# Optimization experiments

Hardware: AMD Instinct MI355X
Metric: run time of the kernel (lower is better)

Reference implementation:

```python
import jax, jax.numpy as jnp
import numpy as np

N, E = 100000, 800000
C_IN, C_OUT, OUT_SIZE = 64, 64, 8


def setup_inputs() -> dict:
    key = jax.random.key(0)
    ks = jax.random.split(key, 20)
    s = 0.05
    def p(k, shape):
        return jax.random.normal(k, shape, jnp.float32) * s
    return {
        "x": jax.random.normal(ks[0], (N, C_IN), jnp.float32),
        "edge_index": jax.random.randint(ks[1], (2, E), 0, N),
        "edge_weight": jax.random.uniform(ks[2], (E,), jnp.float32),
        # GCNConv weights (applied as x @ W), one per gate
        "conv_z_W": p(ks[3], (C_IN, C_OUT)), "conv_z_b": p(ks[4], (C_OUT,)),
        "conv_r_W": p(ks[5], (C_IN, C_OUT)), "conv_r_b": p(ks[6], (C_OUT,)),
        "conv_h_W": p(ks[7], (C_IN, C_OUT)), "conv_h_b": p(ks[8], (C_OUT,)),
        # GRU gate linears: Linear(2*C_OUT, C_OUT)
        "lin_z_W": p(ks[9], (2 * C_OUT, C_OUT)), "lin_z_b": p(ks[10], (C_OUT,)),
        "lin_r_W": p(ks[11], (2 * C_OUT, C_OUT)), "lin_r_b": p(ks[12], (C_OUT,)),
        "lin_h_W": p(ks[13], (2 * C_OUT, C_OUT)), "lin_h_b": p(ks[14], (C_OUT,)),
        # output head Linear(C_OUT, OUT_SIZE)
        "head_W": p(ks[15], (C_OUT, OUT_SIZE)), "head_b": p(ks[16], (OUT_SIZE,)),
    }


def _tgcn_forward(x, edge_index, edge_weight,
                  conv_z_W, conv_z_b, conv_r_W, conv_r_b, conv_h_W, conv_h_b,
                  lin_z_W, lin_z_b, lin_r_W, lin_r_b, lin_h_W, lin_h_b,
                  head_W, head_b):
    n = x.shape[0]
    src, dst = edge_index[0], edge_index[1]
    # GCN normalization with self-loops (fill_value = 1)
    loop = jnp.arange(n)
    src_f = jnp.concatenate([src, loop])
    dst_f = jnp.concatenate([dst, loop])
    ew_f = jnp.concatenate([edge_weight, jnp.ones((n,), x.dtype)])
    deg = jax.ops.segment_sum(ew_f, dst_f, num_segments=n)
    deg_safe = jnp.where(deg > 0, deg, 1.0)
    dinv = jnp.where(deg > 0, jax.lax.rsqrt(deg_safe), 0.0)
    norm = dinv[src_f] * ew_f * dinv[dst_f]  # [E + N]

    def gcn(W, b):
        msg = (x @ W)[src_f] * norm[:, None]          # gather + scale
        return jax.ops.segment_sum(msg, dst_f, num_segments=n) + b  # scatter-add

    H = jnp.zeros((n, conv_z_W.shape[1]), x.dtype)
    Z = jax.nn.sigmoid(jnp.concatenate([gcn(conv_z_W, conv_z_b), H], -1) @ lin_z_W + lin_z_b)
    R = jax.nn.sigmoid(jnp.concatenate([gcn(conv_r_W, conv_r_b), H], -1) @ lin_r_W + lin_r_b)
    H_tilde = jnp.tanh(jnp.concatenate([gcn(conv_h_W, conv_h_b), H * R], -1) @ lin_h_W + lin_h_b)
    H = Z * H + (1.0 - Z) * H_tilde
    return jax.nn.relu(H) @ head_W + head_b


def reference(x, edge_index, edge_weight,
              conv_z_W, conv_z_b, conv_r_W, conv_r_b, conv_h_W, conv_h_b,
              lin_z_W, lin_z_b, lin_r_W, lin_r_b, lin_h_W, lin_h_b,
              head_W, head_b):
    return _tgcn_forward(x, edge_index, edge_weight,
                         conv_z_W, conv_z_b, conv_r_W, conv_r_b, conv_h_W, conv_h_b,
                         lin_z_W, lin_z_b, lin_r_W, lin_r_b, lin_h_W, lin_h_b,
                         head_W, head_b)
```

## Files before the change

### kernel.cpp

```cpp
#include <hip/hip_runtime.h>

#define NN 100000
#define NE 800000
#define C 64
#define NB1 391
#define NTILES 3125
#define MAXDEG 40
#define WBITS 15
#define WMASK 32767u
#define WSCALE 32768.0f


__global__ void ell_build(const int* __restrict__ src, const int* __restrict__ dst,
                          const float* __restrict__ ew,
                          unsigned* __restrict__ cnt, unsigned* __restrict__ ell) {
    int e = blockIdx.x * 256 + threadIdx.x;
    if (e >= NE) return;
    int s = src[e], d = dst[e];
    float w = ew[e];
    unsigned w15 = (unsigned)(w * WSCALE + 0.5f);
    if (w15 > WMASK) w15 = WMASK;
    unsigned pos = atomicAdd(&cnt[d], 1u);
    if (pos < MAXDEG) ell[d * MAXDEG + pos] = ((unsigned)s << WBITS) | w15;
}

__global__ void finalize_ell(const unsigned* __restrict__ cnt,
                             const unsigned* __restrict__ ell,
                             float* __restrict__ dinv) {
    int t = blockIdx.x * 256 + threadIdx.x;
    int n = t >> 6, l = t & 63;
    if (n >= NN) return;
    int k = min((int)cnt[n], MAXDEG);
    float w = (l < k) ? (float)(ell[n * MAXDEG + l] & WMASK) * (1.0f / WSCALE) : 0.0f;
    for (int off = 32; off; off >>= 1) w += __shfl_xor(w, off, 64);
    if (l == 0) dinv[n] = rsqrtf(w + 1.0f);
}

__global__ __launch_bounds__(256) void gather_ell(
    const float* __restrict__ x, const float* __restrict__ dinv,
    const unsigned* __restrict__ cnt, const unsigned* __restrict__ ell,
    float* __restrict__ agg) {
    int t = blockIdx.x * 256 + threadIdx.x;
    int n = t >> 6, c = t & 63;
    if (n >= NN) return;
    float di = dinv[n];
    float acc = x[n * C + c] * di * di;
    int k = min((int)cnt[n], MAXDEG);
    const unsigned* base = ell + (size_t)n * MAXDEG;
    int e = 0;
    for (; e + 7 < k; e += 8) {
        uint4 q0 = *(const uint4*)(base + e);
        uint4 q1 = *(const uint4*)(base + e + 4);
        int s0 = q0.x >> WBITS, s1 = q0.y >> WBITS, s2 = q0.z >> WBITS, s3 = q0.w >> WBITS;
        int s4 = q1.x >> WBITS, s5 = q1.y >> WBITS, s6 = q1.z >> WBITS, s7 = q1.w >> WBITS;
        float x0 = x[s0 * C + c], x1 = x[s1 * C + c], x2 = x[s2 * C + c], x3 = x[s3 * C + c];
        float x4 = x[s4 * C + c], x5 = x[s5 * C + c], x6 = x[s6 * C + c], x7 = x[s7 * C + c];
        float d0 = dinv[s0], d1 = dinv[s1], d2 = dinv[s2], d3 = dinv[s3];
        float d4 = dinv[s4], d5 = dinv[s5], d6 = dinv[s6], d7 = dinv[s7];
        acc += x0 * (d0 * (float)(q0.x & WMASK) * (di * (1.0f / WSCALE)));
        acc += x1 * (d1 * (float)(q0.y & WMASK) * (di * (1.0f / WSCALE)));
        acc += x2 * (d2 * (float)(q0.z & WMASK) * (di * (1.0f / WSCALE)));
        acc += x3 * (d3 * (float)(q0.w & WMASK) * (di * (1.0f / WSCALE)));
        acc += x4 * (d4 * (float)(q1.x & WMASK) * (di * (1.0f / WSCALE)));
        acc += x5 * (d5 * (float)(q1.y & WMASK) * (di * (1.0f / WSCALE)));
        acc += x6 * (d6 * (float)(q1.z & WMASK) * (di * (1.0f / WSCALE)));
        acc += x7 * (d7 * (float)(q1.w & WMASK) * (di * (1.0f / WSCALE)));
    }
    if (e + 3 < k) {
        uint4 q0 = *(const uint4*)(base + e);
        int s0 = q0.x >> WBITS, s1 = q0.y >> WBITS, s2 = q0.z >> WBITS, s3 = q0.w >> WBITS;
        float x0 = x[s0 * C + c], x1 = x[s1 * C + c], x2 = x[s2 * C + c], x3 = x[s3 * C + c];
        float d0 = dinv[s0], d1 = dinv[s1], d2 = dinv[s2], d3 = dinv[s3];
        acc += x0 * (d0 * (float)(q0.x & WMASK) * (di * (1.0f / WSCALE)));
        acc += x1 * (d1 * (float)(q0.y & WMASK) * (di * (1.0f / WSCALE)));
        acc += x2 * (d2 * (float)(q0.z & WMASK) * (di * (1.0f / WSCALE)));
        acc += x3 * (d3 * (float)(q0.w & WMASK) * (di * (1.0f / WSCALE)));
        e += 4;
    }
    for (; e < k; ++e) {
        unsigned u = base[e];
        int s = u >> WBITS;
        acc += x[s * C + c] * (dinv[s] * (float)(u & WMASK) * (di * (1.0f / WSCALE)));
    }
    agg[t] = acc;
}


__global__ void count_deg(const int* __restrict__ dst, const float* __restrict__ ew,
                          float* __restrict__ deg, int* __restrict__ cnt) {
    int e = blockIdx.x * blockDim.x + threadIdx.x;
    if (e < NE) {
        int d = dst[e];
        atomicAdd(&deg[d], ew[e]);
        atomicAdd(&cnt[d], 1);
    }
}

__global__ void scan1(const int* __restrict__ cnt, int* __restrict__ row,
                      int* __restrict__ bsum) {
    __shared__ int s[256];
    int tid = threadIdx.x;
    int gid = blockIdx.x * 256 + tid;
    int v = (gid < NN) ? cnt[gid] : 0;
    s[tid] = v;
    for (int off = 1; off < 256; off <<= 1) {
        __syncthreads();
        int t = (tid >= off) ? s[tid - off] : 0;
        __syncthreads();
        s[tid] += t;
    }
    if (gid < NN) row[gid] = s[tid] - v;
    if (tid == 255) bsum[blockIdx.x] = s[255];
}

__global__ void scan2(const int* __restrict__ bsum, int* __restrict__ bo) {
    __shared__ int s[512];
    int tid = threadIdx.x;
    int v = (tid < NB1) ? bsum[tid] : 0;
    s[tid] = v;
    for (int off = 1; off < 512; off <<= 1) {
        __syncthreads();
        int t = (tid >= off) ? s[tid - off] : 0;
        __syncthreads();
        s[tid] += t;
    }
    if (tid < NB1) bo[tid] = s[tid] - v;
}

__global__ void finalize(int* __restrict__ row, const int* __restrict__ bo,
                         int* __restrict__ cursor, const float* __restrict__ deg,
                         float* __restrict__ dinv) {
    int gid = blockIdx.x * 256 + threadIdx.x;
    if (gid < NN) {
        int r = row[gid] + bo[gid >> 8];
        row[gid] = r;
        cursor[gid] = r;
        dinv[gid] = rsqrtf(deg[gid] + 1.0f);
        if (gid == 0) row[NN] = NE;
    }
}

__global__ void bucket(const int* __restrict__ src, const int* __restrict__ dst,
                       const float* __restrict__ ew, const float* __restrict__ dinv,
                       int* __restrict__ cursor, int2* __restrict__ edata) {
    int e = blockIdx.x * 256 + threadIdx.x;
    if (e < NE) {
        int s = src[e], d = dst[e];
        float nrm = dinv[s] * ew[e] * dinv[d];
        int pos = atomicAdd(&cursor[d], 1);
        edata[pos] = make_int2(s, __float_as_int(nrm));
    }
}

__global__ void gather(const float* __restrict__ x, const float* __restrict__ dinv,
                       const int* __restrict__ row, const int2* __restrict__ edata,
                       float* __restrict__ agg) {
    int t = blockIdx.x * 256 + threadIdx.x;
    int n = t >> 6, c = t & 63;
    if (n >= NN) return;
    float di = dinv[n];
    float acc = x[n * C + c] * di * di;
    int e = row[n], end = row[n + 1];
    for (; e + 1 < end; e += 2) {
        int2 e0 = edata[e], e1 = edata[e + 1];
        acc += x[e0.x * C + c] * __int_as_float(e0.y);
        acc += x[e1.x * C + c] * __int_as_float(e1.y);
    }
    if (e < end) {
        int2 e0 = edata[e];
        acc += x[e0.x * C + c] * __int_as_float(e0.y);
    }
    agg[t] = acc;
}

__global__ void fuse_weights(const float* __restrict__ Wz, const float* __restrict__ bz,
                             const float* __restrict__ Lz, const float* __restrict__ lzb,
                             const float* __restrict__ Wh, const float* __restrict__ bh,
                             const float* __restrict__ Lh, const float* __restrict__ lhb,
                             float* __restrict__ WzF, float* __restrict__ bzF,
                             float* __restrict__ WhF, float* __restrict__ bhF) {
    int t = blockIdx.x * blockDim.x + threadIdx.x;
    if (t < 4096) {
        int i = t >> 6, j = t & 63;
        float s = 0.0f;
#pragma unroll 8
        for (int k = 0; k < 64; k++) s += Wz[i * 64 + k] * Lz[k * 64 + j];
        WzF[t] = s;
    } else if (t < 8192) {
        int u = t - 4096;
        int i = u >> 6, j = u & 63;
        float s = 0.0f;
#pragma unroll 8
        for (int k = 0; k < 64; k++) s += Wh[i * 64 + k] * Lh[k * 64 + j];
        WhF[u] = s;
    } else if (t < 8256) {
        int j = t - 8192;
        float s = lzb[j];
#pragma unroll 8
        for (int k = 0; k < 64; k++) s += bz[k] * Lz[k * 64 + j];
        bzF[j] = s;
    } else if (t < 8320) {
        int j = t - 8256;
        float s = lhb[j];
#pragma unroll 8
        for (int k = 0; k < 64; k++) s += bh[k] * Lh[k * 64 + j];
        bhF[j] = s;
    }
}

__global__ __launch_bounds__(256) void gate_head(
    const float* __restrict__ agg,
    const float* __restrict__ WzF, const float* __restrict__ bzF,
    const float* __restrict__ WhF, const float* __restrict__ bhF,
    const float* __restrict__ headW, const float* __restrict__ headb,
    float* __restrict__ out) {
    __shared__ float sWz[4096];
    __shared__ float sWh[4096];
    __shared__ float sHead[512];
    __shared__ float sbz[64], sbh[64], shb[8];
    __shared__ float sAgg[32][64];
    __shared__ float sRh[32][65];

    int tid = threadIdx.x;
    for (int i = tid; i < 4096; i += 256) { sWz[i] = WzF[i]; sWh[i] = WhF[i]; }
    for (int i = tid; i < 512; i += 256) sHead[i] = headW[i];
    if (tid < 64) { sbz[tid] = bzF[tid]; sbh[tid] = bhF[tid]; }
    if (tid < 8) shb[tid] = headb[tid];
    __syncthreads();

    int j = tid & 63;
    int g = tid >> 6;
    int nl = tid >> 3;
    int j8 = tid & 7;

    for (int tIdx = blockIdx.x; tIdx < NTILES; tIdx += gridDim.x) {
        int n0 = tIdx * 32;
        for (int i = tid; i < 32 * 64; i += 256)
            sAgg[i >> 6][i & 63] = agg[n0 * 64 + i];
        __syncthreads();

        float az[8], ah[8];
#pragma unroll
        for (int l = 0; l < 8; l++) { az[l] = sbz[j]; ah[l] = sbh[j]; }
#pragma unroll 8
        for (int k = 0; k < 64; k++) {
            float wz = sWz[k * 64 + j];
            float wh = sWh[k * 64 + j];
#pragma unroll
            for (int l = 0; l < 8; l++) {
                float a = sAgg[g * 8 + l][k];
                az[l] += a * wz;
                ah[l] += a * wh;
            }
        }
#pragma unroll
        for (int l = 0; l < 8; l++) {
            float z = 1.0f / (1.0f + __expf(-az[l]));
            float ac = fminf(fmaxf(ah[l], -15.0f), 15.0f);
            float e2 = __expf(2.0f * ac);
            float ht = (e2 - 1.0f) / (e2 + 1.0f);
            float h = (1.0f - z) * ht;
            sRh[g * 8 + l][j] = fmaxf(h, 0.0f);
        }
        __syncthreads();

        float s = shb[j8];
#pragma unroll 8
        for (int k = 0; k < 64; k++) s += sRh[nl][k] * sHead[k * 8 + j8];
        out[(n0 + nl) * 8 + j8] = s;
        __syncthreads();
    }
}


__global__ void deg_scatter(const int* __restrict__ dst, const float* __restrict__ ew,
                            float* __restrict__ deg) {
    int e = blockIdx.x * blockDim.x + threadIdx.x;
    if (e < NE) atomicAdd(&deg[dst[e]], ew[e]);
}

__global__ void node_init(const float* __restrict__ x, const float* __restrict__ deg,
                          float* __restrict__ dinv, float* __restrict__ agg) {
    int t = blockIdx.x * blockDim.x + threadIdx.x;
    if (t >= NN * C) return;
    int n = t >> 6;
    float d = deg[n] + 1.0f;
    float di = rsqrtf(d);
    if ((t & 63) == 0) dinv[n] = di;
    agg[t] = x[t] * (di * di);
}

__global__ void edge_scatter(const int* __restrict__ src, const int* __restrict__ dst,
                             const float* __restrict__ ew, const float* __restrict__ dinv,
                             const float* __restrict__ x, float* __restrict__ agg) {
    int t = blockIdx.x * blockDim.x + threadIdx.x;
    int e = t >> 6;
    int c = t & 63;
    if (e >= NE) return;
    int s = src[e];
    int d = dst[e];
    float nrm = dinv[s] * ew[e] * dinv[d];
    atomicAdd(&agg[d * C + c], x[s * C + c] * nrm);
}

extern "C" void kernel_launch(void* const* d_in, const int* in_sizes, int n_in,
                              void* d_out, int out_size, void* d_ws, size_t ws_size,
                              hipStream_t stream) {
    const float* x     = (const float*)d_in[0];
    const int*   ei    = (const int*)d_in[1];
    const float* ew    = (const float*)d_in[2];
    const float* Wz    = (const float*)d_in[3];
    const float* bz    = (const float*)d_in[4];
    const float* Wh    = (const float*)d_in[7];
    const float* bh    = (const float*)d_in[8];
    const float* Lz    = (const float*)d_in[9];
    const float* lzb   = (const float*)d_in[10];
    const float* Lh    = (const float*)d_in[13];
    const float* lhb   = (const float*)d_in[14];
    const float* headW = (const float*)d_in[15];
    const float* headb = (const float*)d_in[16];
    float* out = (float*)d_out;

    const int* src = ei;
    const int* dst = ei + NE;

    float* agg    = (float*)d_ws;
    float* dinv   = agg + (size_t)NN * C;
    float* WzF    = dinv + NN;
    float* WhF    = WzF + 4096;
    float* bzF    = WhF + 4096;
    float* bhF    = bzF + 64;
    float* tail   = bhF + 64;

    unsigned* cnt_u = (unsigned*)tail;
    unsigned* ell   = cnt_u + NN;
    size_t need_ell = (size_t)(tail - (float*)d_ws) * 4 + (size_t)NN * 4
                    + (size_t)NN * MAXDEG * 4;

    float* deg    = tail;
    int*   cnt    = (int*)(deg + NN);
    int*   row    = cnt + NN;
    int*   cursor = row + NN + 1;
    int*   bsum   = cursor + NN;
    int*   bo     = bsum + 512;
    int2*  edata  = (int2*)(bo + 512 + 1);
    size_t need_csr  = ((size_t)(bo + 512 + 1 - (int*)d_ws) + 2 * (size_t)NE) * 4;
    size_t need_base = (size_t)((int*)cnt - (int*)d_ws) * 4;

    fuse_weights<<<33, 256, 0, stream>>>(Wz, bz, Lz, lzb, Wh, bh, Lh, lhb,
                                         WzF, bzF, WhF, bhF);

    if (ws_size >= need_ell) {
        hipMemsetAsync(cnt_u, 0, NN * sizeof(unsigned), stream);
        ell_build<<<(NE + 255) / 256, 256, 0, stream>>>(src, dst, ew, cnt_u, ell);
        finalize_ell<<<(NN * 64 + 255) / 256, 256, 0, stream>>>(cnt_u, ell, dinv);
        gather_ell<<<(NN * C) / 256, 256, 0, stream>>>(x, dinv, cnt_u, ell, agg);
        gate_head<<<768, 256, 0, stream>>>(agg, WzF, bzF, WhF, bhF, headW, headb, out);
    } else if (ws_size >= need_csr) {
        hipMemsetAsync(deg, 0, NN * sizeof(float), stream);
        hipMemsetAsync(cnt, 0, NN * sizeof(int), stream);
        count_deg<<<(NE + 255) / 256, 256, 0, stream>>>(dst, ew, deg, cnt);
        scan1<<<NB1, 256, 0, stream>>>(cnt, row, bsum);
        scan2<<<1, 512, 0, stream>>>(bsum, bo);
        finalize<<<NB1, 256, 0, stream>>>(row, bo, cursor, deg, dinv);
        bucket<<<(NE + 255) / 256, 256, 0, stream>>>(src, dst, ew, dinv, cursor, edata);
        gather<<<(NN * C) / 256, 256, 0, stream>>>(x, dinv, row, edata, agg);
        gate_head<<<768, 256, 0, stream>>>(agg, WzF, bzF, WhF, bhF, headW, headb, out);
    } else if (ws_size >= need_base) {
        hipMemsetAsync(deg, 0, NN * sizeof(float), stream);
        deg_scatter<<<(NE + 255) / 256, 256, 0, stream>>>(dst, ew, deg);
        node_init<<<(NN * C + 255) / 256, 256, 0, stream>>>(x, deg, dinv, agg);
        edge_scatter<<<(NE * C) / 256, 256, 0, stream>>>(src, dst, ew, dinv, x, agg);
        gate_head<<<768, 256, 0, stream>>>(agg, WzF, bzF, WhF, bhF, headW, headb, out);
    }
}
```

Before: 255.8 us.

## Gather bf16 copy of node features and fuse prep work into one kernel

Adds a prep kernel that converts x to bf16 and also does the weight fusion and the zeroing of the per-node counters, replacing a separate kernel launch and a memset. The gather then reads 2-byte features instead of 4-byte ones, halving the bytes per random neighbour row fetch. The cost is an extra full pass over x (read 25.6MB, write 12.8MB) plus lower precision in the aggregated features. It also needs more workspace, so the ELL path may fall back if the workspace is too small.

```diff
diff --git a/kernel.cpp b/kernel.cpp
--- a/kernel.cpp
+++ b/kernel.cpp
@@ -9,6 +9,71 @@
 #define WBITS 15
 #define WMASK 32767u
 #define WSCALE 32768.0f
+
+#define PREP_CONV 6250
+#define PREP_FUSE 33
+#define PREP_ZERO 98
+#define PREP_BLOCKS (PREP_CONV + PREP_FUSE + PREP_ZERO)
+
+__device__ __forceinline__ unsigned short f2bf(float f) {
+    unsigned b = __float_as_uint(f);
+    return (unsigned short)((b + 0x7FFFu + ((b >> 16) & 1u)) >> 16);
+}
+__device__ __forceinline__ float bf2f(unsigned short u) {
+    return __uint_as_float((unsigned)u << 16);
+}
+
+__global__ __launch_bounds__(256) void prep(
+    const float* __restrict__ x, unsigned short* __restrict__ xb,
+    const float* __restrict__ Wz, const float* __restrict__ bz,
+    const float* __restrict__ Lz, const float* __restrict__ lzb,
+    const float* __restrict__ Wh, const float* __restrict__ bh,
+    const float* __restrict__ Lh, const float* __restrict__ lhb,
+    float* __restrict__ WzF, float* __restrict__ bzF,
+    float* __restrict__ WhF, float* __restrict__ bhF,
+    unsigned* __restrict__ cnt) {
+    int b = blockIdx.x;
+    if (b < PREP_CONV) {
+        int i = (b * 256 + threadIdx.x) * 4;
+        float4 v = *(const float4*)(x + i);
+        ushort4 o;
+        o.x = f2bf(v.x); o.y = f2bf(v.y); o.z = f2bf(v.z); o.w = f2bf(v.w);
+        *(ushort4*)(xb + i) = o;
+    } else if (b < PREP_CONV + PREP_FUSE) {
+        int t = (b - PREP_CONV) * 256 + threadIdx.x;
+        if (t < 4096) {
+            int i = t >> 6, j = t & 63;
+            float s = 0.0f;
+#pragma unroll 8
+            for (int k = 0; k < 64; k++) s += Wz[i * 64 + k] * Lz[k * 64 + j];
+            WzF[t] = s;
+        } else if (t < 8192) {
+            int u = t - 4096;
+            int i = u >> 6, j = u & 63;
+            float s = 0.0f;
+#pragma unroll 8
+            for (int k = 0; k < 64; k++) s += Wh[i * 64 + k] * Lh[k * 64 + j];
+            WhF[u] = s;
+        } else if (t < 8256) {
+            int j = t - 8192;
+            float s = lzb[j];
+#pragma unroll 8
+            for (int k = 0; k < 64; k++) s += bz[k] * Lz[k * 64 + j];
+            bzF[j] = s;
+        } else if (t < 8320) {
+            int j = t - 8256;
+            float s = lhb[j];
+#pragma unroll 8
+            for (int k = 0; k < 64; k++) s += bh[k] * Lh[k * 64 + j];
+            bhF[j] = s;
+        }
+    } else {
+        int i = ((b - PREP_CONV - PREP_FUSE) * 256 + threadIdx.x) * 4;
+#pragma unroll
+        for (int q = 0; q < 4; q++)
+            if (i + q < NN) cnt[i + q] = 0u;
+    }
+}
 
 
 __global__ void ell_build(const int* __restrict__ src, const int* __restrict__ dst,
@@ -37,14 +102,15 @@
 }
 
 __global__ __launch_bounds__(256) void gather_ell(
-    const float* __restrict__ x, const float* __restrict__ dinv,
+    const unsigned short* __restrict__ xb, const float* __restrict__ dinv,
     const unsigned* __restrict__ cnt, const unsigned* __restrict__ ell,
     float* __restrict__ agg) {
     int t = blockIdx.x * 256 + threadIdx.x;
     int n = t >> 6, c = t & 63;
     if (n >= NN) return;
     float di = dinv[n];
-    float acc = x[n * C + c] * di * di;
+    float wdi = di * (1.0f / WSCALE);
+    float acc = bf2f(xb[n * C + c]) * (di * di);
     int k = min((int)cnt[n], MAXDEG);
     const unsigned* base = ell + (size_t)n * MAXDEG;
     int e = 0;
@@ -53,38 +119,76 @@
         uint4 q1 = *(const uint4*)(base + e + 4);
         int s0 = q0.x >> WBITS, s1 = q0.y >> WBITS, s2 = q0.z >> WBITS, s3 = q0.w >> WBITS;
         int s4 = q1.x >> WBITS, s5 = q1.y >> WBITS, s6 = q1.z >> WBITS, s7 = q1.w >> WBITS;
-        float x0 = x[s0 * C + c], x1 = x[s1 * C + c], x2 = x[s2 * C + c], x3 = x[s3 * C + c];
-        float x4 = x[s4 * C + c], x5 = x[s5 * C + c], x6 = x[s6 * C + c], x7 = x[s7 * C + c];
+        float x0 = bf2f(xb[s0 * C + c]), x1 = bf2f(xb[s1 * C + c]);
+        float x2 = bf2f(xb[s2 * C + c]), x3 = bf2f(xb[s3 * C + c]);
+        float x4 = bf2f(xb[s4 * C + c]), x5 = bf2f(xb[s5 * C + c]);
+        float x6 = bf2f(xb[s6 * C + c]), x7 = bf2f(xb[s7 * C + c]);
         float d0 = dinv[s0], d1 = dinv[s1], d2 = dinv[s2], d3 = dinv[s3];
         float d4 = dinv[s4], d5 = dinv[s5], d6 = dinv[s6], d7 = dinv[s7];
-        acc += x0 * (d0 * (float)(q0.x & WMASK) * (di * (1.0f / WSCALE)));
-        acc += x1 * (d1 * (float)(q0.y & WMASK) * (di * (1.0f / WSCALE)));
-        acc += x2 * (d2 * (float)(q0.z & WMASK) * (di * (1.0f / WSCALE)));
-        acc += x3 * (d3 * (float)(q0.w & WMASK) * (di * (1.0f / WSCALE)));
-        acc += x4 * (d4 * (float)(q1.x & WMASK) * (di * (1.0f / WSCALE)));
-        acc += x5 * (d5 * (float)(q1.y & WMASK) * (di * (1.0f / WSCALE)));
-        acc += x6 * (d6 * (float)(q1.z & WMASK) * (di * (1.0f / WSCALE)));
-        acc += x7 * (d7 * (float)(q1.w & WMASK) * (di * (1.0f / WSCALE)));
+        acc += x0 * (d0 * (float)(q0.x & WMASK) * wdi);
+        acc += x1 * (d1 * (float)(q0.y & WMASK) * wdi);
+        acc += x2 * (d2 * (float)(q0.z & WMASK) * wdi);
+        acc += x3 * (d3 * (float)(q0.w & WMASK) * wdi);
+        acc += x4 * (d4 * (float)(q1.x & WMASK) * wdi);
+        acc += x5 * (d5 * (float)(q1.y & WMASK) * wdi);
+        acc += x6 * (d6 * (float)(q1.z & WMASK) * wdi);
+        acc += x7 * (d7 * (float)(q1.w & WMASK) * wdi);
     }
     if (e + 3 < k) {
         uint4 q0 = *(const uint4*)(base + e);
         int s0 = q0.x >> WBITS, s1 = q0.y >> WBITS, s2 = q0.z >> WBITS, s3 = q0.w >> WBITS;
-        float x0 = x[s0 * C + c], x1 = x[s1 * C + c], x2 = x[s2 * C + c], x3 = x[s3 * C + c];
+        float x0 = bf2f(xb[s0 * C + c]), x1 = bf2f(xb[s1 * C + c]);
+        float x2 = bf2f(xb[s2 * C + c]), x3 = bf2f(xb[s3 * C + c]);
         float d0 = dinv[s0], d1 = dinv[s1], d2 = dinv[s2], d3 = dinv[s3];
-        acc += x0 * (d0 * (float)(q0.x & WMASK) * (di * (1.0f / WSCALE)));
-        acc += x1 * (d1 * (float)(q0.y & WMASK) * (di * (1.0f / WSCALE)));
-        acc += x2 * (d2 * (float)(q0.z & WMASK) * (di * (1.0f / WSCALE)));
-        acc += x3 * (d3 * (float)(q0.w & WMASK) * (di * (1.0f / WSCALE)));
+        acc += x0 * (d0 * (float)(q0.x & WMASK) * wdi);
+        acc += x1 * (d1 * (float)(q0.y & WMASK) * wdi);
+        acc += x2 * (d2 * (float)(q0.z & WMASK) * wdi);
+        acc += x3 * (d3 * (float)(q0.w & WMASK) * wdi);
         e += 4;
     }
     for (; e < k; ++e) {
         unsigned u = base[e];
         int s = u >> WBITS;
-        acc += x[s * C + c] * (dinv[s] * (float)(u & WMASK) * (di * (1.0f / WSCALE)));
+        acc += bf2f(xb[s * C + c]) * (dinv[s] * (float)(u & WMASK) * wdi);
     }
     agg[t] = acc;
 }
 
+
+__global__ void fuse_weights(const float* __restrict__ Wz, const float* __restrict__ bz,
+                             const float* __restrict__ Lz, const float* __restrict__ lzb,
+                             const float* __restrict__ Wh, const float* __restrict__ bh,
+                             const float* __restrict__ Lh, const float* __restrict__ lhb,
+                             float* __restrict__ WzF, float* __restrict__ bzF,
+                             float* __restrict__ WhF, float* __restrict__ bhF) {
+    int t = blockIdx.x * blockDim.x + threadIdx.x;
+    if (t < 4096) {
+        int i = t >> 6, j = t & 63;
+        float s = 0.0f;
+#pragma unroll 8
+        for (int k = 0; k < 64; k++) s += Wz[i * 64 + k] * Lz[k * 64 + j];
+        WzF[t] = s;
+    } else if (t < 8192) {
+        int u = t - 4096;
+        int i = u >> 6, j = u & 63;
+        float s = 0.0f;
+#pragma unroll 8
+        for (int k = 0; k < 64; k++) s += Wh[i * 64 + k] * Lh[k * 64 + j];
+        WhF[u] = s;
+    } else if (t < 8256) {
+        int j = t - 8192;
+        float s = lzb[j];
+#pragma unroll 8
+        for (int k = 0; k < 64; k++) s += bz[k] * Lz[k * 64 + j];
+        bzF[j] = s;
+    } else if (t < 8320) {
+        int j = t - 8256;
+        float s = lhb[j];
+#pragma unroll 8
+        for (int k = 0; k < 64; k++) s += bh[k] * Lh[k * 64 + j];
+        bhF[j] = s;
+    }
+}
 
 __global__ void count_deg(const int* __restrict__ dst, const float* __restrict__ ew,
                           float* __restrict__ deg, int* __restrict__ cnt) {
@@ -171,41 +275,6 @@
         acc += x[e0.x * C + c] * __int_as_float(e0.y);
     }
     agg[t] = acc;
-}
-
-__global__ void fuse_weights(const float* __restrict__ Wz, const float* __restrict__ bz,
-                             const float* __restrict__ Lz, const float* __restrict__ lzb,
-                             const float* __restrict__ Wh, const float* __restrict__ bh,
-                             const float* __restrict__ Lh, const float* __restrict__ lhb,
-                             float* __restrict__ WzF, float* __restrict__ bzF,
-                             float* __restrict__ WhF, float* __restrict__ bhF) {
-    int t = blockIdx.x * blockDim.x + threadIdx.x;
-    if (t < 4096) {
-        int i = t >> 6, j = t & 63;
-        float s = 0.0f;
-#pragma unroll 8
-        for (int k = 0; k < 64; k++) s += Wz[i * 64 + k] * Lz[k * 64 + j];
-        WzF[t] = s;
-    } else if (t < 8192) {
-        int u = t - 4096;
-        int i = u >> 6, j = u & 63;
-        float s = 0.0f;
-#pragma unroll 8
-        for (int k = 0; k < 64; k++) s += Wh[i * 64 + k] * Lh[k * 64 + j];
-        WhF[u] = s;
-    } else if (t < 8256) {
-        int j = t - 8192;
-        float s = lzb[j];
-#pragma unroll 8
-        for (int k = 0; k < 64; k++) s += bz[k] * Lz[k * 64 + j];
-        bzF[j] = s;
-    } else if (t < 8320) {
-        int j = t - 8256;
-        float s = lhb[j];
-#pragma unroll 8
-        for (int k = 0; k < 64; k++) s += bh[k] * Lh[k * 64 + j];
-        bhF[j] = s;
-    }
 }
 
 __global__ __launch_bounds__(256) void gate_head(
@@ -332,10 +401,11 @@
     float* bhF    = bzF + 64;
     float* tail   = bhF + 64;
 
-    unsigned* cnt_u = (unsigned*)tail;
+    unsigned short* xb = (unsigned short*)tail;
+    unsigned* cnt_u = (unsigned*)(xb + (size_t)NN * C);
     unsigned* ell   = cnt_u + NN;
-    size_t need_ell = (size_t)(tail - (float*)d_ws) * 4 + (size_t)NN * 4
-                    + (size_t)NN * MAXDEG * 4;
+    size_t need_ell = (size_t)(tail - (float*)d_ws) * 4 + (size_t)NN * C * 2
+                    + (size_t)NN * 4 + (size_t)NN * MAXDEG * 4;
 
     float* deg    = tail;
     int*   cnt    = (int*)(deg + NN);
@@ -347,16 +417,16 @@
     size_t need_csr  = ((size_t)(bo + 512 + 1 - (int*)d_ws) + 2 * (size_t)NE) * 4;
     size_t need_base = (size_t)((int*)cnt - (int*)d_ws) * 4;
 
-    fuse_weights<<<33, 256, 0, stream>>>(Wz, bz, Lz, lzb, Wh, bh, Lh, lhb,
-                                         WzF, bzF, WhF, bhF);
-
     if (ws_size >= need_ell) {
-        hipMemsetAsync(cnt_u, 0, NN * sizeof(unsigned), stream);
+        prep<<<PREP_BLOCKS, 256, 0, stream>>>(x, xb, Wz, bz, Lz, lzb, Wh, bh, Lh, lhb,
+                                              WzF, bzF, WhF, bhF, cnt_u);
         ell_build<<<(NE + 255) / 256, 256, 0, stream>>>(src, dst, ew, cnt_u, ell);
         finalize_ell<<<(NN * 64 + 255) / 256, 256, 0, stream>>>(cnt_u, ell, dinv);
-        gather_ell<<<(NN * C) / 256, 256, 0, stream>>>(x, dinv, cnt_u, ell, agg);
+        gather_ell<<<(NN * C) / 256, 256, 0, stream>>>(xb, dinv, cnt_u, ell, agg);
         gate_head<<<768, 256, 0, stream>>>(agg, WzF, bzF, WhF, bhF, headW, headb, out);
     } else if (ws_size >= need_csr) {
+        fuse_weights<<<33, 256, 0, stream>>>(Wz, bz, Lz, lzb, Wh, bh, Lh, lhb,
+                                             WzF, bzF, WhF, bhF);
         hipMemsetAsync(deg, 0, NN * sizeof(float), stream);
         hipMemsetAsync(cnt, 0, NN * sizeof(int), stream);
         count_deg<<<(NE + 255) / 256, 256, 0, stream>>>(dst, ew, deg, cnt);
@@ -367,6 +437,8 @@
         gather<<<(NN * C) / 256, 256, 0, stream>>>(x, dinv, row, edata, agg);
         gate_head<<<768, 256, 0, stream>>>(agg, WzF, bzF, WhF, bhF, headW, headb, out);
     } else if (ws_size >= need_base) {
+        fuse_weights<<<33, 256, 0, stream>>>(Wz, bz, Lz, lzb, Wh, bh, Lh, lhb,
+                                             WzF, bzF, WhF, bhF);
         hipMemsetAsync(deg, 0, NN * sizeof(float), stream);
         deg_scatter<<<(NE + 255) / 256, 256, 0, stream>>>(dst, ew, deg);
         node_init<<<(NN * C + 255) / 256, 256, 0, stream>>>(x, deg, dinv, agg);
```

New measurement: 254.5 us. About the same (-0.5%).
